# Performance work log

Hardware: AMD Instinct MI355X
Metric: run time of the kernel (lower is better)

Reference implementation:

```python
import jax, jax.numpy as jnp
import numpy as np

N_NODES = 50000
N_EDGES = 800000
NEG_SLOPE = 0.2  # GATConv default
BN_EPS = 1e-5


def _seg_softmax(logits, seg, n):
    # per-target-node softmax over incoming edges (PyG softmax w/ +1e-16)
    m = jax.ops.segment_max(logits, seg, num_segments=n)
    m = jnp.where(jnp.isfinite(m), m, 0.0)
    e = jnp.exp(logits - m[seg])
    s = jax.ops.segment_sum(e, seg, num_segments=n)
    return e / (s[seg] + 1e-16)


def _gat_conv(x, src, dst, W, a_src, a_dst, b, concat):
    # x: [N, Fin]; W: [Fin, H*C]; a_src/a_dst: [H, C]
    n = x.shape[0]
    H, C = a_src.shape
    h = (x @ W).reshape(n, H, C)
    al_s = jnp.einsum('nhc,hc->nh', h, a_src)
    al_d = jnp.einsum('nhc,hc->nh', h, a_dst)
    logits = jax.nn.leaky_relu(al_s[src] + al_d[dst], NEG_SLOPE)  # [E, H]
    alpha = _seg_softmax(logits, dst, n)                           # [E, H]
    out = jax.ops.segment_sum(h[src] * alpha[:, :, None], dst, num_segments=n)
    out = out.reshape(n, H * C) if concat else out.mean(axis=1)
    return out + b


def _bn(x, g, b):
    mu = jnp.mean(x, axis=0)
    var = jnp.mean((x - mu) ** 2, axis=0)
    return (x - mu) * jax.lax.rsqrt(var + BN_EPS) * g + b


def _gat_params(key, fin, heads, ch, scale=0.1):
    k1, k2, k3 = jax.random.split(key, 3)
    W = jax.random.normal(k1, (fin, heads * ch), jnp.float32) * scale
    a_s = jax.random.normal(k2, (heads, ch), jnp.float32) * scale
    a_d = jax.random.normal(k3, (heads, ch), jnp.float32) * scale
    return W, a_s, a_d


def setup_inputs() -> dict:
    key = jax.random.key(0)
    ks = jax.random.split(key, 12)
    inp = {}
    inp['x'] = jax.random.normal(ks[0], (N_NODES, 3), jnp.float32)
    inp['edge_index'] = jax.random.randint(ks[1], (2, N_EDGES), 0, N_NODES, jnp.int64 if jax.config.jax_enable_x64 else jnp.int32)
    inp['W11'], inp['as11'], inp['ad11'] = _gat_params(ks[2], 3, 8, 8)
    inp['b11'] = jnp.zeros((64,), jnp.float32)
    inp['W12'], inp['as12'], inp['ad12'] = _gat_params(ks[3], 64, 8, 8)
    inp['b12'] = jnp.zeros((64,), jnp.float32)
    inp['g1'] = jnp.ones((64,), jnp.float32)
    inp['be1'] = jnp.zeros((64,), jnp.float32)
    inp['W21'], inp['as21'], inp['ad21'] = _gat_params(ks[4], 64, 8, 32)
    inp['b21'] = jnp.zeros((256,), jnp.float32)
    inp['W22'], inp['as22'], inp['ad22'] = _gat_params(ks[5], 256, 8, 32)
    inp['b22'] = jnp.zeros((256,), jnp.float32)
    inp['g2'] = jnp.ones((256,), jnp.float32)
    inp['be2'] = jnp.zeros((256,), jnp.float32)
    inp['W31'], inp['as31'], inp['ad31'] = _gat_params(ks[6], 256, 8, 64)
    inp['b31'] = jnp.zeros((512,), jnp.float32)
    inp['W32'], inp['as32'], inp['ad32'] = _gat_params(ks[7], 512, 8, 1)
    inp['b32'] = jnp.zeros((1,), jnp.float32)
    return inp


def reference(x, edge_index,
              W11, as11, ad11, b11, W12, as12, ad12, b12, g1, be1,
              W21, as21, ad21, b21, W22, as22, ad22, b22, g2, be2,
              W31, as31, ad31, b31, W32, as32, ad32, b32):
    n = x.shape[0]
    loops = jnp.arange(n, dtype=edge_index.dtype)
    src = jnp.concatenate([edge_index[0], loops])  # add_self_loops=True
    dst = jnp.concatenate([edge_index[1], loops])
    # GAT(3, 64, 2): conv -> relu -> conv
    h = jax.nn.relu(_gat_conv(x, src, dst, W11, as11, ad11, b11, True))
    h = _gat_conv(h, src, dst, W12, as12, ad12, b12, True)
    h = jax.nn.leaky_relu(_bn(h, g1, be1), 0.1)
    # GAT(64, 256, 2)
    h = jax.nn.relu(_gat_conv(h, src, dst, W21, as21, ad21, b21, True))
    h = _gat_conv(h, src, dst, W22, as22, ad22, b22, True)
    h = jax.nn.leaky_relu(_bn(h, g2, be2), 0.1)
    # GAT(256, 512, 2, 1): conv -> relu -> conv(concat=False)
    h = jax.nn.relu(_gat_conv(h, src, dst, W31, as31, ad31, b31, True))
    h = _gat_conv(h, src, dst, W32, as32, ad32, b32, False)
    return jax.nn.sigmoid(h)
```

## Files before the change

### kernel.cpp

```cpp
#include <hip/hip_runtime.h>
#include <math.h>

typedef short short8 __attribute__((ext_vector_type(8)));
typedef short short4v __attribute__((ext_vector_type(4)));
typedef float f32x4 __attribute__((ext_vector_type(4)));

__device__ __forceinline__ unsigned short f2bf(float v){
  unsigned u = __builtin_bit_cast(unsigned, v);
  u += 0x7FFFu + ((u >> 16) & 1u);
  return (unsigned short)(u >> 16);
}
__device__ __forceinline__ float bf2f(unsigned short b){
  unsigned u = ((unsigned)b) << 16;
  return __builtin_bit_cast(float, u);
}

__global__ void k_deg_prep(const int* __restrict__ dstv, int* __restrict__ deg, int E,
                           const float* __restrict__ W11, const float* __restrict__ W12,
                           const float* __restrict__ W21, const float* __restrict__ W22,
                           const float* __restrict__ W31,
                           unsigned short* __restrict__ bh, unsigned short* __restrict__ bl){
  int i = blockIdx.x*blockDim.x + threadIdx.x;
  if (i < E) atomicAdd(&deg[dstv[i]], 1);
  if (i < 221184){
    const float* W; int K, kpsh, off, Nn;
    if (i < 4096)       { W=W11; K=3;   kpsh=6; off=0;     Nn=64;  }
    else if (i < 8192)  { W=W12; K=64;  kpsh=6; off=4096;  Nn=64;  }
    else if (i < 24576) { W=W21; K=64;  kpsh=6; off=8192;  Nn=256; }
    else if (i < 90112) { W=W22; K=256; kpsh=8; off=24576; Nn=256; }
    else                { W=W31; K=256; kpsh=8; off=90112; Nn=512; }
    int j = i - off;
    int Kp = 1 << kpsh;
    int n = j >> kpsh, k = j & (Kp-1);
    float v = (k < K) ? W[(size_t)k*Nn + n] : 0.0f;
    unsigned short h = f2bf(v);
    bh[i] = h;
    bl[i] = f2bf(v - bf2f(h));
  }
}

__global__ void k_scan(const int* __restrict__ deg, int* __restrict__ off,
                       int* __restrict__ cursor, int N){
  __shared__ int wpre[16];
  __shared__ int s_tot;
  __shared__ int carry;
  int tid = threadIdx.x;
  int lane = tid & 63, wv = tid >> 6;
  if (tid == 0) carry = 0;
  __syncthreads();
  for (int base = 0; base < N; base += 1024){
    int i = base + tid;
    int v = (i < N) ? deg[i] : 0;
    int incl = v;
    #pragma unroll
    for (int d = 1; d < 64; d <<= 1){
      int t = __shfl_up(incl, d, 64);
      if (lane >= d) incl += t;
    }
    if (lane == 63) wpre[wv] = incl;
    __syncthreads();
    if (tid < 16){
      int x = wpre[tid];
      int ix = x;
      #pragma unroll
      for (int d = 1; d < 16; d <<= 1){
        int t = __shfl_up(ix, d, 16);
        if (tid >= d) ix += t;
      }
      wpre[tid] = ix - x;
      if (tid == 15) s_tot = ix;
    }
    __syncthreads();
    int c = carry;
    int excl = c + wpre[wv] + (incl - v);
    if (i < N){ off[i+1] = excl + v; cursor[i] = excl; }
    __syncthreads();
    if (tid == 0) carry = c + s_tot;
    __syncthreads();
  }
  if (tid == 0) off[0] = 0;
}

__global__ void k_fill(const int* __restrict__ srcv, const int* __restrict__ dstv,
                       int* __restrict__ cursor, int* __restrict__ csr, int E){
  int e = blockIdx.x*blockDim.x + threadIdx.x;
  if (e < E){
    int d = dstv[e];
    int p = atomicAdd(&cursor[d], 1);
    csr[p] = srcv[e];
  }
}

__global__ __launch_bounds__(256)
void k_bn_stats(const unsigned short* __restrict__ x, float* __restrict__ psum,
                float* __restrict__ psq, int N, int HC){
  int f   = threadIdx.x & (HC-1);
  int sub = threadIdx.x / HC;
  int subs = 256 / HC;
  int slot = blockIdx.x*subs + sub;
  int stride = gridDim.x*subs;
  float s = 0.f, q = 0.f;
  for (int r = slot; r < N; r += stride){
    float v = bf2f(x[(size_t)r*HC + f]);
    s += v; q += v*v;
  }
  psum[(size_t)slot*HC + f] = s;
  psq [(size_t)slot*HC + f] = q;
}

__global__ __launch_bounds__(256)
void k_bn_coef(const float* __restrict__ psum, const float* __restrict__ psq,
               const float* __restrict__ g, const float* __restrict__ b,
               float* __restrict__ sc, float* __restrict__ sh,
               float invN, int HC, int nb){
  int f = blockIdx.x;
  int t = threadIdx.x;
  float s = 0.f, q = 0.f;
  for (int r = t; r < nb; r += 256){
    s += psum[(size_t)r*HC + f];
    q += psq [(size_t)r*HC + f];
  }
  #pragma unroll
  for (int d = 1; d < 64; d <<= 1){
    s += __shfl_xor(s, d, 64);
    q += __shfl_xor(q, d, 64);
  }
  __shared__ float ss[4], qq[4];
  int wv = t >> 6, ln = t & 63;
  if (ln == 0){ ss[wv] = s; qq[wv] = q; }
  __syncthreads();
  if (t == 0){
    s = ss[0]+ss[1]+ss[2]+ss[3];
    q = qq[0]+qq[1]+qq[2]+qq[3];
    float mu  = s*invN;
    float var = q*invN - mu*mu;
    float rs  = rsqrtf(var + 1e-5f) * g[f];
    sc[f] = rs;
    sh[f] = b[f] - mu*rs;
  }
}

template<int BN, int AFMT>
__global__ __launch_bounds__((BN==64)?256:512)
void gemm_mfma(const void* __restrict__ Av, const unsigned short* __restrict__ Bh,
               const unsigned short* __restrict__ Bl,
               const float* __restrict__ bnsc, const float* __restrict__ bnsh,
               const float* __restrict__ a_s, const float* __restrict__ a_d,
               unsigned short* __restrict__ Pb, float* __restrict__ Ds,
               float* __restrict__ Dd, int M, int K){
  constexpr int WAVES   = (BN==64) ? 4 : 8;
  constexpr int BLOCK   = WAVES*64;
  constexpr int WAVES_N = BN/64;
  constexpr int WAVES_M = WAVES/WAVES_N;
  constexpr int WM      = 64/WAVES_M;
  constexpr int MF      = WM/16;
  constexpr int CH      = (BN==512)?64 : (BN==256)?32 : 8;
  constexpr int TERMS   = (AFMT==2) ? 2 : 3;
  const int Kp = (K + 63) & ~(int)63;

  __shared__ char lds[(TERMS==3)?16384:8192];

  int tid  = threadIdx.x;
  int lane = tid & 63;
  int wid  = tid >> 6;
  int wn = wid % WAVES_N;
  int wm = wid / WAVES_N;
  int n0w = wn*64;
  int wm0 = wm*WM;
  int m0 = blockIdx.x * 64;

  f32x4 acc[MF][4];
  #pragma unroll
  for (int i = 0; i < MF; ++i)
    #pragma unroll
    for (int j = 0; j < 4; ++j)
      acc[i][j] = (f32x4){0.f,0.f,0.f,0.f};

  constexpr int SITER = 512/BLOCK;

  for (int k0 = 0; k0 < Kp; k0 += 64){
    __syncthreads();
    #pragma unroll
    for (int it = 0; it < SITER; ++it){
      int i = it*BLOCK + tid;
      int row = i >> 3, c8 = i & 7;
      int gm = m0 + row;
      int gk = k0 + c8*8;
      int off = row*128 + ((c8 ^ (row&7))<<4);
      if constexpr (AFMT == 2){
        short8 hv = {0,0,0,0,0,0,0,0};
        if (gm < M) hv = *(const short8*)((const unsigned short*)Av + (size_t)gm*K + gk);
        *(short8*)(lds + off) = hv;
      } else if constexpr (AFMT == 1){
        short8 raw = {0,0,0,0,0,0,0,0};
        if (gm < M) raw = *(const short8*)((const unsigned short*)Av + (size_t)gm*K + gk);
        short8 hi, lo;
        #pragma unroll
        for (int j=0;j<8;++j){
          float u = bf2f((unsigned short)raw[j])*bnsc[gk+j] + bnsh[gk+j];
          u = u > 0.f ? u : 0.1f*u;
          if (gm >= M) u = 0.f;
          unsigned short hb = f2bf(u);
          hi[j] = (short)hb;
          lo[j] = (short)f2bf(u - bf2f(hb));
        }
        *(short8*)(lds + off) = hi;
        *(short8*)(lds + 8192 + off) = lo;
      } else {
        const float* A = (const float*)Av;
        float v[8];
        if (gm < M && gk + 8 <= K){
          const float* ap = A + (size_t)gm*K + gk;
          float4 x0 = *(const float4*)ap;
          float4 x1 = *(const float4*)(ap+4);
          v[0]=x0.x; v[1]=x0.y; v[2]=x0.z; v[3]=x0.w;
          v[4]=x1.x; v[5]=x1.y; v[6]=x1.z; v[7]=x1.w;
        } else {
          #pragma unroll
          for (int j=0;j<8;++j){
            int gkj = gk + j;
            v[j] = (gm < M && gkj < K) ? A[(size_t)gm*K + gkj] : 0.0f;
          }
        }
        short8 hi, lo;
        #pragma unroll
        for (int j=0;j<8;++j){
          unsigned short hb = f2bf(v[j]);
          hi[j] = (short)hb;
          lo[j] = (short)f2bf(v[j] - bf2f(hb));
        }
        *(short8*)(lds + off) = hi;
        *(short8*)(lds + 8192 + off) = lo;
      }
    }
    __syncthreads();
    #pragma unroll
    for (int kk = 0; kk < 2; ++kk){
      short8 bhf[4], blf[4];
      #pragma unroll
      for (int nf = 0; nf < 4; ++nf){
        int ncol = n0w + nf*16 + (lane & 15);
        int kidx = k0 + kk*32 + ((lane>>4)<<3);
        size_t bo = (size_t)ncol*Kp + kidx;
        bhf[nf] = *(const short8*)(Bh + bo);
        blf[nf] = *(const short8*)(Bl + bo);
      }
      #pragma unroll
      for (int mt = 0; mt < MF; ++mt){
        int row = wm0 + mt*16 + (lane & 15);
        int c8 = kk*4 + (lane>>4);
        int off = row*128 + ((c8 ^ (row&7))<<4);
        short8 ah = *(const short8*)(lds + off);
        #pragma unroll
        for (int nf = 0; nf < 4; ++nf){
          acc[mt][nf] = __builtin_amdgcn_mfma_f32_16x16x32_bf16(ah, bhf[nf], acc[mt][nf], 0,0,0);
          acc[mt][nf] = __builtin_amdgcn_mfma_f32_16x16x32_bf16(ah, blf[nf], acc[mt][nf], 0,0,0);
        }
        if constexpr (TERMS == 3){
          short8 al = *(const short8*)(lds + 8192 + off);
          #pragma unroll
          for (int nf = 0; nf < 4; ++nf)
            acc[mt][nf] = __builtin_amdgcn_mfma_f32_16x16x32_bf16(al, bhf[nf], acc[mt][nf], 0,0,0);
        }
      }
    }
  }

  float asv[4], adv[4];
  #pragma unroll
  for (int nf=0; nf<4; ++nf){
    int gcol = n0w + nf*16 + (lane&15);
    asv[nf] = a_s[gcol];
    adv[nf] = a_d[gcol];
  }
  #pragma unroll
  for (int mt = 0; mt < MF; ++mt){
    #pragma unroll
    for (int r = 0; r < 4; ++r){
      int gm = m0 + wm0 + mt*16 + ((lane>>4)<<2) + r;
      bool ok = gm < M;
      #pragma unroll
      for (int nf=0;nf<4;++nf){
        if (ok) Pb[(size_t)gm*BN + n0w + nf*16 + (lane&15)] = f2bf(acc[mt][nf][r]);
      }
      if constexpr (CH == 64){
        float ps = acc[mt][0][r]*asv[0] + acc[mt][1][r]*asv[1]
                 + acc[mt][2][r]*asv[2] + acc[mt][3][r]*asv[3];
        float pd = acc[mt][0][r]*adv[0] + acc[mt][1][r]*adv[1]
                 + acc[mt][2][r]*adv[2] + acc[mt][3][r]*adv[3];
        #pragma unroll
        for (int d2=1; d2<16; d2<<=1){ ps += __shfl_xor(ps,d2,64); pd += __shfl_xor(pd,d2,64); }
        if (ok && (lane&15)==0){
          int head = n0w >> 6;
          Ds[(size_t)gm*8 + head] = ps;
          Dd[(size_t)gm*8 + head] = pd;
        }
      } else if constexpr (CH == 32){
        float ps0 = acc[mt][0][r]*asv[0] + acc[mt][1][r]*asv[1];
        float ps1 = acc[mt][2][r]*asv[2] + acc[mt][3][r]*asv[3];
        float pd0 = acc[mt][0][r]*adv[0] + acc[mt][1][r]*adv[1];
        float pd1 = acc[mt][2][r]*adv[2] + acc[mt][3][r]*adv[3];
        #pragma unroll
        for (int d2=1; d2<16; d2<<=1){
          ps0 += __shfl_xor(ps0,d2,64); ps1 += __shfl_xor(ps1,d2,64);
          pd0 += __shfl_xor(pd0,d2,64); pd1 += __shfl_xor(pd1,d2,64);
        }
        if (ok && (lane&15)==0){
          int head = n0w >> 5;
          Ds[(size_t)gm*8 + head]     = ps0;
          Ds[(size_t)gm*8 + head + 1] = ps1;
          Dd[(size_t)gm*8 + head]     = pd0;
          Dd[(size_t)gm*8 + head + 1] = pd1;
        }
      } else {
        #pragma unroll
        for (int nf=0;nf<4;++nf){
          float ps = acc[mt][nf][r]*asv[nf];
          float pd = acc[mt][nf][r]*adv[nf];
          #pragma unroll
          for (int d2=1; d2<8; d2<<=1){ ps += __shfl_xor(ps,d2,64); pd += __shfl_xor(pd,d2,64); }
          if (ok && (lane&7)==0){
            int head = nf*2 + ((lane>>3)&1);
            Ds[(size_t)gm*8 + head] = ps;
            Dd[(size_t)gm*8 + head] = pd;
          }
        }
      }
    }
  }
}

template<int HC, int ACT>
__global__ __launch_bounds__(256)
void k_agg(const unsigned short* __restrict__ Pb, const float* __restrict__ Ds,
           const float* __restrict__ Dd, const int* __restrict__ off,
           const int* __restrict__ csr, const float* __restrict__ bias,
           unsigned short* __restrict__ outb, int N){
  __shared__ float salpha[4][512];
  int lane = threadIdx.x & 63;
  int wid  = threadIdx.x >> 6;
  int n = blockIdx.x*4 + wid;
  if (n >= N) return;
  int o0 = off[n], deg = off[n+1]-o0;

  float aldn[8];
  {
    const float* dn = Dd + (unsigned)n*8u;
    float4 x0 = *(const float4*)dn;
    float4 x1 = *(const float4*)(dn+4);
    aldn[0]=x0.x; aldn[1]=x0.y; aldn[2]=x0.z; aldn[3]=x0.w;
    aldn[4]=x1.x; aldn[5]=x1.y; aldn[6]=x1.z; aldn[7]=x1.w;
  }

  if (deg < 64){
    int nE = deg + 1;
    int myidx = (lane < deg) ? csr[o0+lane] : n;
    bool active = (lane < nE);
    float v[8];
    {
      const float* dp = Ds + (unsigned)myidx*8u;
      float4 x0 = *(const float4*)dp;
      float4 x1 = *(const float4*)(dp+4);
      float t[8] = {x0.x,x0.y,x0.z,x0.w,x1.x,x1.y,x1.z,x1.w};
      #pragma unroll
      for (int h=0;h<8;++h){
        float u = t[h] + aldn[h];
        u = u > 0.f ? u : 0.2f*u;
        v[h] = active ? u : -1e30f;
      }
    }
    float m[8];
    #pragma unroll
    for (int h=0;h<8;++h) m[h]=v[h];
    #pragma unroll
    for (int d=1; d<64; d<<=1)
      #pragma unroll
      for (int h=0;h<8;++h) m[h] = fmaxf(m[h], __shfl_xor(m[h], d, 64));
    float sv[8], s[8];
    #pragma unroll
    for (int h=0;h<8;++h){ sv[h] = active ? __expf(v[h]-m[h]) : 0.f; s[h]=sv[h]; }
    #pragma unroll
    for (int d=1; d<64; d<<=1)
      #pragma unroll
      for (int h=0;h<8;++h) s[h] += __shfl_xor(s[h], d, 64);
    if (active){
      #pragma unroll
      for (int h=0;h<8;++h) salpha[wid][lane*8+h] = sv[h] / (s[h] + 1e-16f);
    }
    asm volatile("s_waitcnt lgkmcnt(0)" ::: "memory");

    if constexpr (HC == 512){
      int myh = lane >> 3;
      float acc[8] = {0,0,0,0,0,0,0,0};
      const unsigned short* Pl = Pb + lane*8;
      for (int e=0; e<nE; ++e){
        int src = __shfl(myidx, e, 64);
        float alpha = salpha[wid][e*8 + myh];
        short8 w = *(const short8*)(Pl + (unsigned)src*512u);
        #pragma unroll
        for (int j=0;j<8;++j) acc[j] += alpha * bf2f((unsigned short)w[j]);
      }
      #pragma unroll
      for (int j=0;j<8;++j){
        int f = lane*8 + j;
        float u = acc[j] + bias[f];
        if (ACT == 1) u = fmaxf(u, 0.0f);
        outb[(unsigned)n*512u + f] = f2bf(u);
      }
    } else if constexpr (HC == 256){
      int sub = lane >> 5, fl = lane & 31;
      int h = fl >> 2;
      float acc[8] = {0,0,0,0,0,0,0,0};
      const unsigned short* Pl = Pb + fl*8;
      for (int e=0; e<nE; e+=2){
        int eg = e + sub;
        bool val = eg < nE;
        int src = __shfl(myidx, val ? eg : 0, 64);
        float alpha = val ? salpha[wid][eg*8 + h] : 0.f;
        short8 w = *(const short8*)(Pl + (unsigned)src*256u);
        #pragma unroll
        for (int j=0;j<8;++j) acc[j] += alpha * bf2f((unsigned short)w[j]);
      }
      #pragma unroll
      for (int j=0;j<8;++j) acc[j] += __shfl_xor(acc[j], 32, 64);
      if (sub == 0){
        short8 ov;
        #pragma unroll
        for (int j=0;j<8;++j){
          int f = fl*8 + j;
          float u = acc[j] + bias[f];
          if (ACT == 1) u = fmaxf(u, 0.0f);
          ov[j] = (short)f2bf(u);
        }
        *(short8*)(outb + (unsigned)n*256u + fl*8) = ov;
      }
    } else {
      int sub = lane >> 4, fl = lane & 15;
      int h = fl >> 1;
      float acc[4] = {0,0,0,0};
      const unsigned short* Pl = Pb + fl*4;
      for (int e=0; e<nE; e+=4){
        int eg = e + sub;
        bool val = eg < nE;
        int src = __shfl(myidx, val ? eg : 0, 64);
        float alpha = val ? salpha[wid][eg*8 + h] : 0.f;
        short4v w = *(const short4v*)(Pl + (unsigned)src*64u);
        #pragma unroll
        for (int j=0;j<4;++j) acc[j] += alpha * bf2f((unsigned short)w[j]);
      }
      #pragma unroll
      for (int j=0;j<4;++j){
        acc[j] += __shfl_xor(acc[j], 16, 64);
        acc[j] += __shfl_xor(acc[j], 32, 64);
      }
      if (sub == 0){
        short4v ov;
        #pragma unroll
        for (int j=0;j<4;++j){
          int f = fl*4 + j;
          float u = acc[j] + bias[f];
          if (ACT == 1) u = fmaxf(u, 0.0f);
          ov[j] = (short)f2bf(u);
        }
        *(short4v*)(outb + (unsigned)n*64u + fl*4) = ov;
      }
    }
  } else {
    constexpr int R = HC/64;
    int myh = lane >> 3;
    float m[8];
    #pragma unroll
    for (int h=0;h<8;++h) m[h] = -1e30f;
    for (int e = lane; e <= deg; e += 64){
      int src = (e < deg) ? csr[o0+e] : n;
      const float* ap = Ds + (size_t)src*8;
      #pragma unroll
      for (int h=0;h<8;++h){
        float u = ap[h] + aldn[h];
        u = u > 0.f ? u : 0.2f*u;
        m[h] = fmaxf(m[h], u);
      }
    }
    #pragma unroll
    for (int d=1; d<64; d<<=1)
      #pragma unroll
      for (int h=0;h<8;++h) m[h] = fmaxf(m[h], __shfl_xor(m[h], d, 64));
    float s[8] = {0,0,0,0,0,0,0,0};
    for (int e = lane; e <= deg; e += 64){
      int src = (e < deg) ? csr[o0+e] : n;
      const float* ap = Ds + (size_t)src*8;
      #pragma unroll
      for (int h=0;h<8;++h){
        float u = ap[h] + aldn[h];
        u = u > 0.f ? u : 0.2f*u;
        s[h] += __expf(u - m[h]);
      }
    }
    #pragma unroll
    for (int d=1; d<64; d<<=1)
      #pragma unroll
      for (int h=0;h<8;++h) s[h] += __shfl_xor(s[h], d, 64);
    float mh = m[myh];
    float rsh = 1.0f/(s[myh] + 1e-16f);
    float adh = aldn[myh];
    float acc[R];
    #pragma unroll
    for (int j=0;j<R;++j) acc[j]=0.f;
    for (int e = 0; e <= deg; ++e){
      int src = (e < deg) ? csr[o0+e] : n;
      float u = Ds[(size_t)src*8 + myh] + adh;
      u = u > 0.f ? u : 0.2f*u;
      float alpha = __expf(u - mh) * rsh;
      const unsigned short* hp = Pb + (size_t)src*HC + lane*R;
      if constexpr (R == 1){
        acc[0] += alpha * bf2f(hp[0]);
      } else if constexpr (R == 4){
        short4v w = *(const short4v*)hp;
        #pragma unroll
        for (int j=0;j<4;++j) acc[j] += alpha * bf2f((unsigned short)w[j]);
      } else {
        short8 w = *(const short8*)hp;
        #pragma unroll
        for (int j=0;j<8;++j) acc[j] += alpha * bf2f((unsigned short)w[j]);
      }
    }
    #pragma unroll
    for (int j = 0; j < R; ++j){
      int f = lane*R + j;
      float u = acc[j] + bias[f];
      if (ACT == 1) u = fmaxf(u, 0.0f);
      outb[(size_t)n*HC + f] = f2bf(u);
    }
  }
}

__global__ __launch_bounds__(256)
void gemm8(const unsigned short* __restrict__ Qb, const float* __restrict__ W,
           float* __restrict__ h8, int M){
  int lane = threadIdx.x & 63;
  int gw = (blockIdx.x*blockDim.x + threadIdx.x) >> 6;
  int nw = (gridDim.x*blockDim.x) >> 6;
  float w[8][8];
  const float* wp = W + lane*64;
  #pragma unroll
  for (int j=0;j<8;++j){
    float4 a = *(const float4*)(wp + j*8);
    float4 b = *(const float4*)(wp + j*8 + 4);
    w[j][0]=a.x; w[j][1]=a.y; w[j][2]=a.z; w[j][3]=a.w;
    w[j][4]=b.x; w[j][5]=b.y; w[j][6]=b.z; w[j][7]=b.w;
  }
  for (int n = gw; n < M; n += nw){
    short8 v8 = *(const short8*)(Qb + (size_t)n*512 + lane*8);
    float p[8] = {0,0,0,0,0,0,0,0};
    #pragma unroll
    for (int j=0;j<8;++j){
      float x = bf2f((unsigned short)v8[j]);
      #pragma unroll
      for (int o=0;o<8;++o) p[o] += x * w[j][o];
    }
    #pragma unroll
    for (int d=1; d<64; d<<=1)
      #pragma unroll
      for (int o=0;o<8;++o) p[o] += __shfl_xor(p[o], d, 64);
    if (lane == 0){
      float4 y0 = make_float4(p[0],p[1],p[2],p[3]);
      float4 y1 = make_float4(p[4],p[5],p[6],p[7]);
      *(float4*)(h8 + (size_t)n*8)     = y0;
      *(float4*)(h8 + (size_t)n*8 + 4) = y1;
    }
  }
}

__global__ __launch_bounds__(256)
void k_final(const float* __restrict__ h8, const float* __restrict__ a_s,
             const float* __restrict__ a_d, const int* __restrict__ off,
             const int* __restrict__ csr, const float* __restrict__ b32,
             float* __restrict__ outp, int N){
  int lane = threadIdx.x & 63;
  int wv   = threadIdx.x >> 6;
  int n = blockIdx.x*4 + wv;
  if (n >= N) return;
  int o0 = off[n], deg = off[n+1]-o0;
  float asv[8], adv[8];
  #pragma unroll
  for (int h=0;h<8;++h){ asv[h]=a_s[h]; adv[h]=a_d[h]; }
  float aldn[8];
  {
    const float* hp = h8 + (size_t)n*8;
    float4 x0 = *(const float4*)hp;
    float4 x1 = *(const float4*)(hp+4);
    float hn[8] = {x0.x,x0.y,x0.z,x0.w,x1.x,x1.y,x1.z,x1.w};
    #pragma unroll
    for (int h=0;h<8;++h) aldn[h] = hn[h]*adv[h];
  }

  if (deg < 64){
    int nE = deg + 1;
    int src = (lane < deg) ? csr[o0+lane] : n;
    bool act = (lane < nE);
    float hs[8];
    {
      const float* hp = h8 + (size_t)src*8;
      float4 x0 = *(const float4*)hp;
      float4 x1 = *(const float4*)(hp+4);
      hs[0]=x0.x; hs[1]=x0.y; hs[2]=x0.z; hs[3]=x0.w;
      hs[4]=x1.x; hs[5]=x1.y; hs[6]=x1.z; hs[7]=x1.w;
    }
    float v[8];
    #pragma unroll
    for (int h=0;h<8;++h){
      float u = hs[h]*asv[h] + aldn[h];
      u = u > 0.f ? u : 0.2f*u;
      v[h] = act ? u : -1e30f;
    }
    float m[8];
    #pragma unroll
    for (int h=0;h<8;++h) m[h]=v[h];
    #pragma unroll
    for (int d=1; d<64; d<<=1)
      #pragma unroll
      for (int h=0;h<8;++h) m[h] = fmaxf(m[h], __shfl_xor(m[h], d, 64));
    float s[8], t[8];
    #pragma unroll
    for (int h=0;h<8;++h){
      float e = act ? __expf(v[h]-m[h]) : 0.f;
      s[h]=e; t[h]=e*hs[h];
    }
    #pragma unroll
    for (int d=1; d<64; d<<=1)
      #pragma unroll
      for (int h=0;h<8;++h){
        s[h] += __shfl_xor(s[h], d, 64);
        t[h] += __shfl_xor(t[h], d, 64);
      }
    if (lane == 0){
      float o = 0.f;
      #pragma unroll
      for (int h=0;h<8;++h) o += t[h]/(s[h]+1e-16f);
      o = o*0.125f + b32[0];
      outp[n] = 1.0f/(1.0f + __expf(-o));
    }
  } else if (lane == 0){
    float m[8], s[8], agg[8];
    #pragma unroll
    for (int h=0;h<8;++h){ m[h]=-1e30f; s[h]=0.f; agg[h]=0.f; }
    for (int e = 0; e <= deg; ++e){
      int src = (e < deg) ? csr[o0+e] : n;
      #pragma unroll
      for (int h=0;h<8;++h){
        float u = h8[(size_t)src*8+h]*asv[h] + aldn[h];
        u = u > 0.f ? u : 0.2f*u;
        m[h] = fmaxf(m[h], u);
      }
    }
    for (int e = 0; e <= deg; ++e){
      int src = (e < deg) ? csr[o0+e] : n;
      #pragma unroll
      for (int h=0;h<8;++h){
        float u = h8[(size_t)src*8+h]*asv[h] + aldn[h];
        u = u > 0.f ? u : 0.2f*u;
        float ex = __expf(u - m[h]);
        s[h] += ex;
        agg[h] += ex * h8[(size_t)src*8+h];
      }
    }
    float o = 0.f;
    #pragma unroll
    for (int h=0;h<8;++h) o += agg[h]/(s[h]+1e-16f);
    o = o*0.125f + b32[0];
    outp[n] = 1.0f/(1.0f + __expf(-o));
  }
}

extern "C" void kernel_launch(void* const* d_in, const int* in_sizes, int n_in,
                              void* d_out, int out_size, void* d_ws, size_t ws_size,
                              hipStream_t stream){
  int N = in_sizes[0]/3;
  int E = in_sizes[1]/2;
  const float* x    = (const float*)d_in[0];
  const int*   ei   = (const int*)  d_in[1];
  const float* W11  = (const float*)d_in[2];
  const float* as11 = (const float*)d_in[3];
  const float* ad11 = (const float*)d_in[4];
  const float* b11  = (const float*)d_in[5];
  const float* W12  = (const float*)d_in[6];
  const float* as12 = (const float*)d_in[7];
  const float* ad12 = (const float*)d_in[8];
  const float* b12  = (const float*)d_in[9];
  const float* g1   = (const float*)d_in[10];
  const float* be1  = (const float*)d_in[11];
  const float* W21  = (const float*)d_in[12];
  const float* as21 = (const float*)d_in[13];
  const float* ad21 = (const float*)d_in[14];
  const float* b21  = (const float*)d_in[15];
  const float* W22  = (const float*)d_in[16];
  const float* as22 = (const float*)d_in[17];
  const float* ad22 = (const float*)d_in[18];
  const float* b22  = (const float*)d_in[19];
  const float* g2   = (const float*)d_in[20];
  const float* be2  = (const float*)d_in[21];
  const float* W31  = (const float*)d_in[22];
  const float* as31 = (const float*)d_in[23];
  const float* ad31 = (const float*)d_in[24];
  const float* b31  = (const float*)d_in[25];
  const float* W32  = (const float*)d_in[26];
  const float* as32 = (const float*)d_in[27];
  const float* ad32 = (const float*)d_in[28];
  const float* b32  = (const float*)d_in[29];

  char* ws = (char*)d_ws;
  size_t o = 0;
  auto alloc = [&](size_t bytes)->char*{
    char* p = ws + o;
    o = (o + bytes + 255) & ~(size_t)255;
    return p;
  };
  int*   deg    = (int*)  alloc((size_t)N*4);
  int*   off    = (int*)  alloc((size_t)(N+1)*4);
  int*   cursor = (int*)  alloc((size_t)N*4);
  int*   csr    = (int*)  alloc((size_t)E*4);
  unsigned short* bh = (unsigned short*)alloc(221184*2);
  unsigned short* bl = (unsigned short*)alloc(221184*2);
  float* h8     = (float*)alloc((size_t)N*8*4);
  float* psum   = (float*)alloc(1024*64*4);
  float* psq    = (float*)alloc(1024*64*4);
  float* bnsc   = (float*)alloc(1024);
  float* bnsh   = (float*)alloc(1024);
  unsigned short* Pb = (unsigned short*)alloc((size_t)N*512*2);
  unsigned short* Qb = (unsigned short*)alloc((size_t)N*512*2);
  float* Dsb    = (float*)alloc((size_t)N*8*4);
  float* Ddb    = (float*)alloc((size_t)N*8*4);
  (void)ws_size;

  const int BT11=0, BT12=4096, BT21=8192, BT22=24576, BT31=90112;

  hipMemsetAsync(deg, 0, (size_t)N*4, stream);
  int eb = (E+255)/256;
  k_deg_prep<<<eb, 256, 0, stream>>>(ei+E, deg, E, W11, W12, W21, W22, W31, bh, bl);
  k_scan<<<1, 1024, 0, stream>>>(deg, off, cursor, N);
  k_fill<<<eb, 256, 0, stream>>>(ei, ei+E, cursor, csr, E);

  int mb = (N+63)/64;
  int nb4 = (N+3)/4;
  float invN = 1.0f/(float)N;

  gemm_mfma<64,0><<<mb, 256, 0, stream>>>(x, bh+BT11, bl+BT11, nullptr, nullptr,
                                          as11, ad11, Pb, Dsb, Ddb, N, 3);
  k_agg<64,1><<<nb4, 256, 0, stream>>>(Pb, Dsb, Ddb, off, csr, b11, Qb, N);

  gemm_mfma<64,2><<<mb, 256, 0, stream>>>(Qb, bh+BT12, bl+BT12, nullptr, nullptr,
                                          as12, ad12, Pb, Dsb, Ddb, N, 64);
  k_agg<64,0><<<nb4, 256, 0, stream>>>(Pb, Dsb, Ddb, off, csr, b12, Qb, N);
  k_bn_stats<<<256, 256, 0, stream>>>(Qb, psum, psq, N, 64);
  k_bn_coef<<<64, 256, 0, stream>>>(psum, psq, g1, be1, bnsc, bnsh, invN, 64, 1024);

  gemm_mfma<256,1><<<mb, 512, 0, stream>>>(Qb, bh+BT21, bl+BT21, bnsc, bnsh,
                                           as21, ad21, Pb, Dsb, Ddb, N, 64);
  k_agg<256,1><<<nb4, 256, 0, stream>>>(Pb, Dsb, Ddb, off, csr, b21, Qb, N);

  gemm_mfma<256,2><<<mb, 512, 0, stream>>>(Qb, bh+BT22, bl+BT22, nullptr, nullptr,
                                           as22, ad22, Pb, Dsb, Ddb, N, 256);
  k_agg<256,0><<<nb4, 256, 0, stream>>>(Pb, Dsb, Ddb, off, csr, b22, Qb, N);
  k_bn_stats<<<256, 256, 0, stream>>>(Qb, psum, psq, N, 256);
  k_bn_coef<<<256, 256, 0, stream>>>(psum, psq, g2, be2, bnsc, bnsh, invN, 256, 256);

  gemm_mfma<512,1><<<mb, 512, 0, stream>>>(Qb, bh+BT31, bl+BT31, bnsc, bnsh,
                                           as31, ad31, Pb, Dsb, Ddb, N, 256);
  k_agg<512,1><<<nb4, 256, 0, stream>>>(Pb, Dsb, Ddb, off, csr, b31, Qb, N);

  gemm8<<<1024, 256, 0, stream>>>(Qb, W32, h8, N);
  k_final<<<nb4, 256, 0, stream>>>(h8, as32, ad32, off, csr, b32,
                                   (float*)d_out, N);
}
```

Baseline: 1.067 ms.

## Parallelize CSR degree scan, drop A-lo split for BN input, widen 64-feature aggregation

Replaces the single-block serial prefix scan over node degrees with a three-kernel multi-block scan (block scans, scan of block sums, add-back). Drops the low-order bf16 correction term for the BN-normalized GEMM input (AFMT 1), halving its LDS staging and MFMA terms at some precision cost. Changes the 64-channel aggregation path to load 8 bf16 per lane, processing 8 edges per iteration with one extra shuffle reduction. The new scan adds two extra kernel launches.

```diff
diff --git a/kernel.cpp b/kernel.cpp
--- a/kernel.cpp
+++ b/kernel.cpp
@@ -39,46 +39,60 @@
   }
 }
 
-__global__ void k_scan(const int* __restrict__ deg, int* __restrict__ off,
-                       int* __restrict__ cursor, int N){
+__global__ __launch_bounds__(1024)
+void k_scan1(const int* __restrict__ deg, int* __restrict__ off,
+             int* __restrict__ bsum, int N){
   __shared__ int wpre[16];
-  __shared__ int s_tot;
-  __shared__ int carry;
   int tid = threadIdx.x;
   int lane = tid & 63, wv = tid >> 6;
-  if (tid == 0) carry = 0;
+  int i = blockIdx.x*1024 + tid;
+  int v = (i < N) ? deg[i] : 0;
+  int incl = v;
+  #pragma unroll
+  for (int d = 1; d < 64; d <<= 1){
+    int t = __shfl_up(incl, d, 64);
+    if (lane >= d) incl += t;
+  }
+  if (lane == 63) wpre[wv] = incl;
   __syncthreads();
-  for (int base = 0; base < N; base += 1024){
-    int i = base + tid;
-    int v = (i < N) ? deg[i] : 0;
-    int incl = v;
-    #pragma unroll
-    for (int d = 1; d < 64; d <<= 1){
-      int t = __shfl_up(incl, d, 64);
-      if (lane >= d) incl += t;
-    }
-    if (lane == 63) wpre[wv] = incl;
-    __syncthreads();
-    if (tid < 16){
-      int x = wpre[tid];
-      int ix = x;
-      #pragma unroll
-      for (int d = 1; d < 16; d <<= 1){
-        int t = __shfl_up(ix, d, 16);
-        if (tid >= d) ix += t;
-      }
-      wpre[tid] = ix - x;
-      if (tid == 15) s_tot = ix;
-    }
-    __syncthreads();
-    int c = carry;
-    int excl = c + wpre[wv] + (incl - v);
-    if (i < N){ off[i+1] = excl + v; cursor[i] = excl; }
-    __syncthreads();
-    if (tid == 0) carry = c + s_tot;
-    __syncthreads();
-  }
-  if (tid == 0) off[0] = 0;
+  if (tid < 16){
+    int x = wpre[tid];
+    int ix = x;
+    #pragma unroll
+    for (int d = 1; d < 16; d <<= 1){
+      int t = __shfl_up(ix, d, 16);
+      if (tid >= d) ix += t;
+    }
+    wpre[tid] = ix - x;
+    if (tid == 15) bsum[blockIdx.x] = ix;
+  }
+  __syncthreads();
+  if (i < N) off[i+1] = wpre[wv] + incl;
+}
+
+__global__ void k_scan2(int* __restrict__ bsum, int* __restrict__ bpre, int nb){
+  int t = threadIdx.x;
+  int v = (t < nb) ? bsum[t] : 0;
+  int incl = v;
+  #pragma unroll
+  for (int d = 1; d < 64; d <<= 1){
+    int u = __shfl_up(incl, d, 64);
+    if (t >= d) incl += u;
+  }
+  if (t < nb) bpre[t] = incl - v;
+}
+
+__global__ __launch_bounds__(1024)
+void k_scan3(const int* __restrict__ deg, int* __restrict__ off,
+             const int* __restrict__ bpre, int* __restrict__ cursor, int N){
+  int i = blockIdx.x*1024 + threadIdx.x;
+  if (i < N){
+    int base = bpre[blockIdx.x];
+    int incl = off[i+1] + base;
+    off[i+1] = incl;
+    cursor[i] = incl - deg[i];
+    if (i == 0) off[0] = 0;
+  }
 }
 
 __global__ void k_fill(const int* __restrict__ srcv, const int* __restrict__ dstv,
@@ -155,7 +169,7 @@
   constexpr int WM      = 64/WAVES_M;
   constexpr int MF      = WM/16;
   constexpr int CH      = (BN==512)?64 : (BN==256)?32 : 8;
-  constexpr int TERMS   = (AFMT==2) ? 2 : 3;
+  constexpr int TERMS   = (AFMT==0) ? 3 : 2;
   const int Kp = (K + 63) & ~(int)63;
 
   __shared__ char lds[(TERMS==3)?16384:8192];
@@ -194,18 +208,15 @@
       } else if constexpr (AFMT == 1){
         short8 raw = {0,0,0,0,0,0,0,0};
         if (gm < M) raw = *(const short8*)((const unsigned short*)Av + (size_t)gm*K + gk);
-        short8 hi, lo;
+        short8 hi;
         #pragma unroll
         for (int j=0;j<8;++j){
           float u = bf2f((unsigned short)raw[j])*bnsc[gk+j] + bnsh[gk+j];
           u = u > 0.f ? u : 0.1f*u;
           if (gm >= M) u = 0.f;
-          unsigned short hb = f2bf(u);
-          hi[j] = (short)hb;
-          lo[j] = (short)f2bf(u - bf2f(hb));
+          hi[j] = (short)f2bf(u);
         }
         *(short8*)(lds + off) = hi;
-        *(short8*)(lds + 8192 + off) = lo;
       } else {
         const float* A = (const float*)Av;
         float v[8];
@@ -435,34 +446,34 @@
         *(short8*)(outb + (unsigned)n*256u + fl*8) = ov;
       }
     } else {
-      int sub = lane >> 4, fl = lane & 15;
-      int h = fl >> 1;
-      float acc[4] = {0,0,0,0};
-      const unsigned short* Pl = Pb + fl*4;
-      for (int e=0; e<nE; e+=4){
+      int sub = lane >> 3, fl = lane & 7;
+      float acc[8] = {0,0,0,0,0,0,0,0};
+      const unsigned short* Pl = Pb + fl*8;
+      for (int e=0; e<nE; e+=8){
         int eg = e + sub;
         bool val = eg < nE;
         int src = __shfl(myidx, val ? eg : 0, 64);
-        float alpha = val ? salpha[wid][eg*8 + h] : 0.f;
-        short4v w = *(const short4v*)(Pl + (unsigned)src*64u);
-        #pragma unroll
-        for (int j=0;j<4;++j) acc[j] += alpha * bf2f((unsigned short)w[j]);
-      }
-      #pragma unroll
-      for (int j=0;j<4;++j){
+        float alpha = val ? salpha[wid][eg*8 + fl] : 0.f;
+        short8 w = *(const short8*)(Pl + (unsigned)src*64u);
+        #pragma unroll
+        for (int j=0;j<8;++j) acc[j] += alpha * bf2f((unsigned short)w[j]);
+      }
+      #pragma unroll
+      for (int j=0;j<8;++j){
+        acc[j] += __shfl_xor(acc[j], 8, 64);
         acc[j] += __shfl_xor(acc[j], 16, 64);
         acc[j] += __shfl_xor(acc[j], 32, 64);
       }
       if (sub == 0){
-        short4v ov;
-        #pragma unroll
-        for (int j=0;j<4;++j){
-          int f = fl*4 + j;
+        short8 ov;
+        #pragma unroll
+        for (int j=0;j<8;++j){
+          int f = fl*8 + j;
           float u = acc[j] + bias[f];
           if (ACT == 1) u = fmaxf(u, 0.0f);
           ov[j] = (short)f2bf(u);
         }
-        *(short4v*)(outb + (unsigned)n*64u + fl*4) = ov;
+        *(short8*)(outb + (unsigned)n*64u + fl*8) = ov;
       }
     }
   } else {
@@ -719,6 +730,8 @@
   int*   off    = (int*)  alloc((size_t)(N+1)*4);
   int*   cursor = (int*)  alloc((size_t)N*4);
   int*   csr    = (int*)  alloc((size_t)E*4);
+  int*   bsum   = (int*)  alloc(64*4);
+  int*   bpre   = (int*)  alloc(64*4);
   unsigned short* bh = (unsigned short*)alloc(221184*2);
   unsigned short* bl = (unsigned short*)alloc(221184*2);
   float* h8     = (float*)alloc((size_t)N*8*4);
@@ -736,8 +749,11 @@
 
   hipMemsetAsync(deg, 0, (size_t)N*4, stream);
   int eb = (E+255)/256;
+  int nb1k = (N+1023)/1024;
   k_deg_prep<<<eb, 256, 0, stream>>>(ei+E, deg, E, W11, W12, W21, W22, W31, bh, bl);
-  k_scan<<<1, 1024, 0, stream>>>(deg, off, cursor, N);
+  k_scan1<<<nb1k, 1024, 0, stream>>>(deg, off, bsum, N);
+  k_scan2<<<1, 64, 0, stream>>>(bsum, bpre, nb1k);
+  k_scan3<<<nb1k, 1024, 0, stream>>>(deg, off, bpre, cursor, N);
   k_fill<<<eb, 256, 0, stream>>>(ei, ei+E, cursor, csr, E);
 
   int mb = (N+63)/64;
```

New measurement: 1.031 ms, median of 2. -3.4%, faster.
